# Optimization experiments

Hardware: AMD Instinct MI355X
Metric: run time of the kernel (lower is better)

The kernel has to match this reference:

```python
import jax, jax.numpy as jnp
import numpy as np
import math

B, S, HID, H = 1, 2048, 1024, 16
D = HID // H  # head_dim = 64


def setup_inputs() -> dict:
    key = jax.random.key(0)
    ks = jax.random.split(key, 12)
    s = 0.02
    x = jax.random.normal(ks[0], (B, S, HID), jnp.float32)
    Wq = jax.random.normal(ks[1], (HID, HID), jnp.float32) * s
    bq = jnp.zeros((HID,), jnp.float32)
    Wk = jax.random.normal(ks[2], (HID, HID), jnp.float32) * s
    bk = jnp.zeros((HID,), jnp.float32)
    Wv = jax.random.normal(ks[3], (HID, HID), jnp.float32) * s
    bv = jnp.zeros((HID,), jnp.float32)
    Wo = jax.random.normal(ks[4], (HID, HID), jnp.float32) * s
    bo = jnp.zeros((HID,), jnp.float32)
    # nn.Parameter(torch.ones(3,3)) at init; small noise so the bias is non-degenerate
    cmw = jnp.ones((3, 3), jnp.float32) + 0.1 * jax.random.normal(ks[5], (3, 3), jnp.float32)
    # full causal [B,S,S] mask so the mask.shape[1]==seq_len branch is taken
    mask = jnp.tril(jnp.ones((B, S, S), jnp.int32))
    modality_info = jax.random.randint(ks[6], (B, S), 0, 3, dtype=jnp.int64)
    return dict(x=x, Wq=Wq, bq=bq, Wk=Wk, bk=bk, Wv=Wv, bv=bv, Wo=Wo, bo=bo,
                cmw=cmw, mask=mask, modality_info=modality_info)


def reference(x, Wq, bq, Wk, bk, Wv, bv, Wo, bo, cmw, mask, modality_info):
    b, s, _ = x.shape
    # QKV projections (torch Linear: y = x @ W.T + b), split into heads [B,H,S,D]
    q = (x @ Wq.T + bq).reshape(b, s, H, D).transpose(0, 2, 1, 3)
    k = (x @ Wk.T + bk).reshape(b, s, H, D).transpose(0, 2, 1, 3)
    v = (x @ Wv.T + bv).reshape(b, s, H, D).transpose(0, 2, 1, 3)
    scores = jnp.einsum('bhqd,bhkd->bhqk', q, k) / math.sqrt(D)  # [B,H,S,S]
    # cross-modal bias: gather from 3x3 table via pairwise modality indices -> [B,S,S]
    bias = cmw[modality_info[:, :, None], modality_info[:, None, :]]
    scores = scores + bias[:, None, :, :]  # equals original broadcast when B==1
    scores = jnp.where(mask[:, None, :, :] == 0, -1e9, scores)
    attn = jax.nn.softmax(scores, axis=-1)  # dropout is identity in eval
    ctx = jnp.einsum('bhqk,bhkd->bhqd', attn, v)          # [B,H,S,D]
    ctx = ctx.transpose(0, 2, 1, 3).reshape(b, s, HID)    # [B,S,HID]
    return ctx @ Wo.T + bo
```

## Files before the change

kernel.cpp:

```cpp
#include <hip/hip_runtime.h>
#include <hip/hip_bf16.h>
#include <math.h>

#define S_LEN 2048
#define HID   1024
#define NHEAD 16

using bf16x8 = __attribute__((ext_vector_type(8))) short;
using f32x4  = __attribute__((ext_vector_type(4))) float;

__device__ __forceinline__ float bf2f(short s) {
  union { unsigned u; float f; } c;
  c.u = ((unsigned)(unsigned short)s) << 16;
  return c.f;
}
__device__ __forceinline__ short f2bf(float f) {
  union { float f; unsigned u; } c; c.f = f;
  unsigned u = c.u;
  unsigned r = (u + 0x7fffu + ((u >> 16) & 1u)) >> 16;
  return (short)r;
}
__device__ __forceinline__ float loadf(const void* base, long idx, int is_bf) {
  return is_bf ? bf2f(((const short*)base)[idx]) : ((const float*)base)[idx];
}

__global__ void detect_kernel(const unsigned* __restrict__ xw,
                              const int* __restrict__ modw,
                              int* __restrict__ flags) {
  const int t = threadIdx.x;
  int cnt = 0;
  for (int i = t; i < 1024; i += 64) {
    const unsigned fld = (xw[i] >> 7) & 0xFFu;
    cnt += (fld >= 100u && fld <= 135u) ? 1 : 0;
  }
  int odd = 0;
  for (int i = 0; i < 4; ++i) {
    const int wv = modw[2 * (t + 64 * i) + 1];
    odd += (wv != 0) ? 1 : 0;
  }
  for (int m = 1; m < 64; m <<= 1) {
    cnt += __shfl_xor(cnt, m);
    odd += __shfl_xor(odd, m);
  }
  if (t == 0) {
    flags[0] = (cnt >= 512) ? 1 : 0;
    flags[1] = (odd == 0) ? 1 : 0;
  }
}

__global__ __launch_bounds__(256) void convert5(
    const void* __restrict__ s0, const void* __restrict__ s1, const void* __restrict__ s2,
    const void* __restrict__ s3, const void* __restrict__ s4,
    short* __restrict__ d0, short* __restrict__ d1, short* __restrict__ d2,
    short* __restrict__ d3, short* __restrict__ d4,
    const int* __restrict__ flags) {
  const int a = blockIdx.y;
  const void* src = (a == 0) ? s0 : (a == 1) ? s1 : (a == 2) ? s2 : (a == 3) ? s3 : s4;
  short* dst = (a == 0) ? d0 : (a == 1) ? d1 : (a == 2) ? d2 : (a == 3) ? d3 : d4;
  const long n = (a == 0) ? (2L << 20) : (1L << 20);
  const int is_bf = flags[0];
  long i = (long)(blockIdx.x * 256 + threadIdx.x) * 8;
  const long stride = (long)gridDim.x * 256 * 8;
  if (is_bf) {
    for (; i < n; i += stride)
      *(bf16x8*)(dst + i) = *(const bf16x8*)((const short*)src + i);
  } else {
    for (; i < n; i += stride) {
      const float* p = (const float*)src + i;
      bf16x8 r;
#pragma unroll
      for (int j = 0; j < 8; ++j) r[j] = f2bf(p[j]);
      *(bf16x8*)(dst + i) = r;
    }
  }
}

__global__ __launch_bounds__(256) void gemm_bt3(
    const short* __restrict__ A,
    const short* __restrict__ W0, const short* __restrict__ W1, const short* __restrict__ W2,
    const void* __restrict__ b0, const void* __restrict__ b1, const void* __restrict__ b2,
    void* __restrict__ C0, void* __restrict__ C1, void* __restrict__ C2,
    const int* __restrict__ flags, int nbn, int store_f32)
{
  constexpr int K = 1024;
  constexpr int N = 1024;
  __shared__ short As[128 * 32];
  __shared__ short Bs[128 * 32];

  const int t = threadIdx.x;
  const int w = t >> 6, lane = t & 63;
  const int l15 = lane & 15, quad = lane >> 4;
  const int wm = w >> 1, wn = w & 1;

  const int is_bf = flags[0];
  const int bx = blockIdx.x;
  const int mat = bx / nbn;
  const int n0 = (bx % nbn) * 128;
  const int m0 = blockIdx.y * 128;

  const short* W  = (mat == 0) ? W0 : (mat == 1 ? W1 : W2);
  const void* bia = (mat == 0) ? b0 : (mat == 1 ? b1 : b2);
  void*       C   = (mat == 0) ? C0 : (mat == 1 ? C1 : C2);

  f32x4 acc[4][4];
  for (int mi = 0; mi < 4; ++mi)
    for (int ni = 0; ni < 4; ++ni)
      for (int r = 0; r < 4; ++r) acc[mi][ni][r] = 0.f;

  const int srow = t >> 2;
  const int sch  = (t & 3) * 8;
  const short* Ap = A + (long)(m0 + srow) * K + sch;
  const short* Wp = W + (long)(n0 + srow) * K + sch;

  bf16x8 ra0 = *(const bf16x8*)(Ap);
  bf16x8 ra1 = *(const bf16x8*)(Ap + 64L * K);
  bf16x8 rb0 = *(const bf16x8*)(Wp);
  bf16x8 rb1 = *(const bf16x8*)(Wp + 64L * K);

  for (int kt = 0; kt < K / 32; ++kt) {
    __syncthreads();
    *(bf16x8*)&As[(srow)      * 32 + sch] = ra0;
    *(bf16x8*)&As[(srow + 64) * 32 + sch] = ra1;
    *(bf16x8*)&Bs[(srow)      * 32 + sch] = rb0;
    *(bf16x8*)&Bs[(srow + 64) * 32 + sch] = rb1;
    __syncthreads();
    if (kt + 1 < K / 32) {
      ra0 = *(const bf16x8*)(Ap + (kt + 1) * 32);
      ra1 = *(const bf16x8*)(Ap + (kt + 1) * 32 + 64L * K);
      rb0 = *(const bf16x8*)(Wp + (kt + 1) * 32);
      rb1 = *(const bf16x8*)(Wp + (kt + 1) * 32 + 64L * K);
    }
    bf16x8 af[4], bfr[4];
    for (int mi = 0; mi < 4; ++mi)
      af[mi] = *(const bf16x8*)&As[(wm * 64 + mi * 16 + l15) * 32 + quad * 8];
    for (int ni = 0; ni < 4; ++ni)
      bfr[ni] = *(const bf16x8*)&Bs[(wn * 64 + ni * 16 + l15) * 32 + quad * 8];
    for (int mi = 0; mi < 4; ++mi)
      for (int ni = 0; ni < 4; ++ni)
        acc[mi][ni] = __builtin_amdgcn_mfma_f32_16x16x32_bf16(af[mi], bfr[ni], acc[mi][ni], 0, 0, 0);
  }

  for (int ni = 0; ni < 4; ++ni) {
    const int col = n0 + wn * 64 + ni * 16 + l15;
    const float bv = loadf(bia, col, is_bf);
    for (int mi = 0; mi < 4; ++mi) {
      const int row = m0 + wm * 64 + mi * 16 + quad * 4;
      for (int r = 0; r < 4; ++r) {
        const float v = acc[mi][ni][r] + bv;
        const long idx = (long)(row + r) * N + col;
        if (store_f32) ((float*)C)[idx] = v;
        else           ((short*)C)[idx] = f2bf(v);
      }
    }
  }
}

__global__ __launch_bounds__(256) void attn_kernel(
    const short* __restrict__ Q, const short* __restrict__ Kg, const short* __restrict__ Vg,
    const int* __restrict__ mod, const void* __restrict__ cmw,
    const int* __restrict__ flags, short* __restrict__ CTX)
{
  __shared__ short Ks[64 * 80];
  __shared__ short Vt[64 * 80];
  __shared__ short Ps[4 * 16 * 80];
  __shared__ float cm[9];
  __shared__ int mods[2048];

  const int t = threadIdx.x;
  const int w = t >> 6, lane = t & 63;
  const int l15 = lane & 15, quad = lane >> 4;
  const int h = blockIdx.y;
  const int m64 = flags[1];

  if (t < 9) cm[t] = loadf(cmw, t, flags[0]);
  for (int i = t; i < 2048; i += 256) mods[i] = mod[i << m64];
  __syncthreads();

  const int krow = t >> 3, kch = (t & 7) * 8;
  const int vkp = t & 63, vdc = (t >> 6) * 8;

  for (int half = 0; half < 2; ++half) {
    const int strip = (half == 0) ? (int)blockIdx.x : 31 - (int)blockIdx.x;
    const int q0 = strip * 64;
    const int nkt = strip + 1;

    const short* qb = Q + (long)(q0 + w * 16 + l15) * HID + h * 64 + quad * 8;
    const bf16x8 aq0 = *(const bf16x8*)qb;
    const bf16x8 aq1 = *(const bf16x8*)(qb + 32);

    int mrow[4];
    for (int r = 0; r < 4; ++r) mrow[r] = mods[q0 + w * 16 + quad * 4 + r];

    float m_i[4], l_i[4];
    f32x4 acc_o[4];
    for (int r = 0; r < 4; ++r) { m_i[r] = -1e30f; l_i[r] = 0.f; }
    for (int ni = 0; ni < 4; ++ni)
      for (int r = 0; r < 4; ++r) acc_o[ni][r] = 0.f;

    bf16x8 rk0 = *(const bf16x8*)(Kg + (long)krow * HID + h * 64 + kch);
    bf16x8 rk1 = *(const bf16x8*)(Kg + (long)(krow + 32) * HID + h * 64 + kch);
    bf16x8 rv0 = *(const bf16x8*)(Vg + (long)vkp * HID + h * 64 + vdc);
    bf16x8 rv1 = *(const bf16x8*)(Vg + (long)vkp * HID + h * 64 + 32 + vdc);

    for (int kt = 0; kt < nkt; ++kt) {
      __syncthreads();
      *(bf16x8*)&Ks[krow * 80 + kch] = rk0;
      *(bf16x8*)&Ks[(krow + 32) * 80 + kch] = rk1;
#pragma unroll
      for (int j = 0; j < 8; ++j) Vt[(vdc + j) * 80 + vkp] = rv0[j];
#pragma unroll
      for (int j = 0; j < 8; ++j) Vt[(vdc + 32 + j) * 80 + vkp] = rv1[j];
      __syncthreads();
      if (kt + 1 < nkt) {
        const long kb = (long)((kt + 1) * 64) * HID + h * 64;
        rk0 = *(const bf16x8*)(Kg + kb + (long)krow * HID + kch);
        rk1 = *(const bf16x8*)(Kg + kb + (long)(krow + 32) * HID + kch);
        rv0 = *(const bf16x8*)(Vg + kb + (long)vkp * HID + vdc);
        rv1 = *(const bf16x8*)(Vg + kb + (long)vkp * HID + 32 + vdc);
      }

      f32x4 sc[4];
      for (int nt = 0; nt < 4; ++nt) {
        const bf16x8 kb0 = *(const bf16x8*)&Ks[(nt * 16 + l15) * 80 + quad * 8];
        const bf16x8 kb1 = *(const bf16x8*)&Ks[(nt * 16 + l15) * 80 + 32 + quad * 8];
        f32x4 z;
        for (int r = 0; r < 4; ++r) z[r] = 0.f;
        z = __builtin_amdgcn_mfma_f32_16x16x32_bf16(aq0, kb0, z, 0, 0, 0);
        z = __builtin_amdgcn_mfma_f32_16x16x32_bf16(aq1, kb1, z, 0, 0, 0);
        sc[nt] = z;
      }

      float sv[4][4], rmax[4];
      for (int r = 0; r < 4; ++r) rmax[r] = -1e30f;
      for (int nt = 0; nt < 4; ++nt) {
        const int mcol = mods[kt * 64 + nt * 16 + l15];
        for (int r = 0; r < 4; ++r) {
          float x = sc[nt][r] * 0.125f + cm[mrow[r] * 3 + mcol];
          sv[nt][r] = x;
          rmax[r] = fmaxf(rmax[r], x);
        }
      }
      if (kt == nkt - 1) {
        for (int r = 0; r < 4; ++r) rmax[r] = -1e30f;
        for (int nt = 0; nt < 4; ++nt) {
          const int col = kt * 64 + nt * 16 + l15;
          for (int r = 0; r < 4; ++r) {
            const int row = q0 + w * 16 + quad * 4 + r;
            sv[nt][r] = (col <= row) ? sv[nt][r] : -1e30f;
            rmax[r] = fmaxf(rmax[r], sv[nt][r]);
          }
        }
      }
      for (int off = 1; off < 16; off <<= 1)
        for (int r = 0; r < 4; ++r) rmax[r] = fmaxf(rmax[r], __shfl_xor(rmax[r], off));

      float alpha[4], rsum[4];
      for (int r = 0; r < 4; ++r) {
        const float mn = fmaxf(m_i[r], rmax[r]);
        alpha[r] = __expf(m_i[r] - mn);
        m_i[r] = mn;
        rsum[r] = 0.f;
      }
      short pb[4][4];
      for (int nt = 0; nt < 4; ++nt)
        for (int r = 0; r < 4; ++r) {
          const float p = __expf(sv[nt][r] - m_i[r]);
          rsum[r] += p;
          pb[nt][r] = f2bf(p);
        }
      for (int off = 1; off < 16; off <<= 1)
        for (int r = 0; r < 4; ++r) rsum[r] += __shfl_xor(rsum[r], off);
      for (int r = 0; r < 4; ++r) l_i[r] = l_i[r] * alpha[r] + rsum[r];
      for (int ni = 0; ni < 4; ++ni)
        for (int r = 0; r < 4; ++r) acc_o[ni][r] *= alpha[r];

      short* Pw = &Ps[w * 16 * 80];
      for (int nt = 0; nt < 4; ++nt)
        for (int r = 0; r < 4; ++r)
          Pw[(quad * 4 + r) * 80 + nt * 16 + l15] = pb[nt][r];
      asm volatile("s_waitcnt lgkmcnt(0)" ::: "memory");

      for (int kk = 0; kk < 2; ++kk) {
        const bf16x8 ap = *(const bf16x8*)&Pw[l15 * 80 + kk * 32 + quad * 8];
        for (int ni = 0; ni < 4; ++ni) {
          const bf16x8 bv = *(const bf16x8*)&Vt[(ni * 16 + l15) * 80 + kk * 32 + quad * 8];
          acc_o[ni] = __builtin_amdgcn_mfma_f32_16x16x32_bf16(ap, bv, acc_o[ni], 0, 0, 0);
        }
      }
    }

    for (int ni = 0; ni < 4; ++ni) {
      const int col = h * 64 + ni * 16 + l15;
      for (int r = 0; r < 4; ++r) {
        const int row = q0 + w * 16 + quad * 4 + r;
        CTX[(long)row * HID + col] = f2bf(acc_o[ni][r] / l_i[r]);
      }
    }
  }
}

extern "C" void kernel_launch(void* const* d_in, const int* in_sizes, int n_in,
                              void* d_out, int out_size, void* d_ws, size_t ws_size,
                              hipStream_t stream) {
  constexpr long M1 = 1024L * 1024L;
  int*   flags = (int*)d_ws;
  short* base  = (short*)d_ws + 128;
  short* xb  = base;
  short* Wqb = xb + 2 * M1;
  short* Wkb = Wqb + M1;
  short* Wvb = Wkb + M1;
  short* Wob = Wvb + M1;
  short* Qw  = Wob + M1;
  short* Kw  = Qw + 2 * M1;
  short* Vw  = Kw + 2 * M1;
  short* CTX = Vw + 2 * M1;
  const int* modality = (const int*)d_in[11];

  detect_kernel<<<1, 64, 0, stream>>>((const unsigned*)d_in[0], modality, flags);
  convert5<<<dim3(512, 5), 256, 0, stream>>>(
      d_in[0], d_in[1], d_in[3], d_in[5], d_in[7],
      xb, Wqb, Wkb, Wvb, Wob, flags);

  gemm_bt3<<<dim3(24, 16), 256, 0, stream>>>(
      xb, Wqb, Wkb, Wvb, d_in[2], d_in[4], d_in[6],
      Qw, Kw, Vw, flags, 8, 0);
  attn_kernel<<<dim3(16, NHEAD), 256, 0, stream>>>(Qw, Kw, Vw, modality, d_in[9], flags, CTX);
  gemm_bt3<<<dim3(8, 16), 256, 0, stream>>>(
      CTX, Wob, Wob, Wob, d_in[8], d_in[8], d_in[8],
      d_out, d_out, d_out, flags, 8, 1);
}
```

Before: 206.8 us.

## Split attention KV range across two blocks with merge pass; shrink GEMM N-tile

```diff
diff --git a/kernel.cpp b/kernel.cpp
--- a/kernel.cpp
+++ b/kernel.cpp
@@ -7,6 +7,7 @@
 #define NHEAD 16
 
 using bf16x8 = __attribute__((ext_vector_type(8))) short;
+using bf16x4 = __attribute__((ext_vector_type(4))) short;
 using f32x4  = __attribute__((ext_vector_type(4))) float;
 
 __device__ __forceinline__ float bf2f(short s) {
@@ -85,7 +86,7 @@
   constexpr int K = 1024;
   constexpr int N = 1024;
   __shared__ short As[128 * 32];
-  __shared__ short Bs[128 * 32];
+  __shared__ short Bs[64 * 32];
 
   const int t = threadIdx.x;
   const int w = t >> 6, lane = t & 63;
@@ -95,16 +96,16 @@
   const int is_bf = flags[0];
   const int bx = blockIdx.x;
   const int mat = bx / nbn;
-  const int n0 = (bx % nbn) * 128;
+  const int n0 = (bx % nbn) * 64;
   const int m0 = blockIdx.y * 128;
 
   const short* W  = (mat == 0) ? W0 : (mat == 1 ? W1 : W2);
   const void* bia = (mat == 0) ? b0 : (mat == 1 ? b1 : b2);
   void*       C   = (mat == 0) ? C0 : (mat == 1 ? C1 : C2);
 
-  f32x4 acc[4][4];
+  f32x4 acc[4][2];
   for (int mi = 0; mi < 4; ++mi)
-    for (int ni = 0; ni < 4; ++ni)
+    for (int ni = 0; ni < 2; ++ni)
       for (int r = 0; r < 4; ++r) acc[mi][ni][r] = 0.f;
 
   const int srow = t >> 2;
@@ -115,33 +116,30 @@
   bf16x8 ra0 = *(const bf16x8*)(Ap);
   bf16x8 ra1 = *(const bf16x8*)(Ap + 64L * K);
   bf16x8 rb0 = *(const bf16x8*)(Wp);
-  bf16x8 rb1 = *(const bf16x8*)(Wp + 64L * K);
 
   for (int kt = 0; kt < K / 32; ++kt) {
     __syncthreads();
     *(bf16x8*)&As[(srow)      * 32 + sch] = ra0;
     *(bf16x8*)&As[(srow + 64) * 32 + sch] = ra1;
     *(bf16x8*)&Bs[(srow)      * 32 + sch] = rb0;
-    *(bf16x8*)&Bs[(srow + 64) * 32 + sch] = rb1;
     __syncthreads();
     if (kt + 1 < K / 32) {
       ra0 = *(const bf16x8*)(Ap + (kt + 1) * 32);
       ra1 = *(const bf16x8*)(Ap + (kt + 1) * 32 + 64L * K);
       rb0 = *(const bf16x8*)(Wp + (kt + 1) * 32);
-      rb1 = *(const bf16x8*)(Wp + (kt + 1) * 32 + 64L * K);
-    }
-    bf16x8 af[4], bfr[4];
+    }
+    bf16x8 af[4], bfr[2];
     for (int mi = 0; mi < 4; ++mi)
       af[mi] = *(const bf16x8*)&As[(wm * 64 + mi * 16 + l15) * 32 + quad * 8];
-    for (int ni = 0; ni < 4; ++ni)
-      bfr[ni] = *(const bf16x8*)&Bs[(wn * 64 + ni * 16 + l15) * 32 + quad * 8];
+    for (int ni = 0; ni < 2; ++ni)
+      bfr[ni] = *(const bf16x8*)&Bs[(wn * 32 + ni * 16 + l15) * 32 + quad * 8];
     for (int mi = 0; mi < 4; ++mi)
-      for (int ni = 0; ni < 4; ++ni)
+      for (int ni = 0; ni < 2; ++ni)
         acc[mi][ni] = __builtin_amdgcn_mfma_f32_16x16x32_bf16(af[mi], bfr[ni], acc[mi][ni], 0, 0, 0);
   }
 
-  for (int ni = 0; ni < 4; ++ni) {
-    const int col = n0 + wn * 64 + ni * 16 + l15;
+  for (int ni = 0; ni < 2; ++ni) {
+    const int col = n0 + wn * 32 + ni * 16 + l15;
     const float bv = loadf(bia, col, is_bf);
     for (int mi = 0; mi < 4; ++mi) {
       const int row = m0 + wm * 64 + mi * 16 + quad * 4;
@@ -155,10 +153,11 @@
   }
 }
 
-__global__ __launch_bounds__(256) void attn_kernel(
+__global__ __launch_bounds__(256) void attn_split(
     const short* __restrict__ Q, const short* __restrict__ Kg, const short* __restrict__ Vg,
     const int* __restrict__ mod, const void* __restrict__ cmw,
-    const int* __restrict__ flags, short* __restrict__ CTX)
+    const int* __restrict__ flags,
+    short* __restrict__ PO, float* __restrict__ PM, float* __restrict__ PL)
 {
   __shared__ short Ks[64 * 80];
   __shared__ short Vt[64 * 80];
@@ -170,6 +169,8 @@
   const int w = t >> 6, lane = t & 63;
   const int l15 = lane & 15, quad = lane >> 4;
   const int h = blockIdx.y;
+  const int pair = blockIdx.x >> 1;
+  const int par  = blockIdx.x & 1;
   const int m64 = flags[1];
 
   if (t < 9) cm[t] = loadf(cmw, t, flags[0]);
@@ -179,8 +180,8 @@
   const int krow = t >> 3, kch = (t & 7) * 8;
   const int vkp = t & 63, vdc = (t >> 6) * 8;
 
-  for (int half = 0; half < 2; ++half) {
-    const int strip = (half == 0) ? (int)blockIdx.x : 31 - (int)blockIdx.x;
+  for (int si = 0; si < 2; ++si) {
+    const int strip = (si == 0) ? pair : 31 - pair;
     const int q0 = strip * 64;
     const int nkt = strip + 1;
 
@@ -197,12 +198,16 @@
     for (int ni = 0; ni < 4; ++ni)
       for (int r = 0; r < 4; ++r) acc_o[ni][r] = 0.f;
 
-    bf16x8 rk0 = *(const bf16x8*)(Kg + (long)krow * HID + h * 64 + kch);
-    bf16x8 rk1 = *(const bf16x8*)(Kg + (long)(krow + 32) * HID + h * 64 + kch);
-    bf16x8 rv0 = *(const bf16x8*)(Vg + (long)vkp * HID + h * 64 + vdc);
-    bf16x8 rv1 = *(const bf16x8*)(Vg + (long)vkp * HID + h * 64 + 32 + vdc);
-
-    for (int kt = 0; kt < nkt; ++kt) {
+    bf16x8 rk0, rk1, rv0, rv1;
+    if (par < nkt) {
+      const long kb = (long)(par * 64) * HID + h * 64;
+      rk0 = *(const bf16x8*)(Kg + kb + (long)krow * HID + kch);
+      rk1 = *(const bf16x8*)(Kg + kb + (long)(krow + 32) * HID + kch);
+      rv0 = *(const bf16x8*)(Vg + kb + (long)vkp * HID + vdc);
+      rv1 = *(const bf16x8*)(Vg + kb + (long)vkp * HID + 32 + vdc);
+    }
+
+    for (int kt = par; kt < nkt; kt += 2) {
       __syncthreads();
       *(bf16x8*)&Ks[krow * 80 + kch] = rk0;
       *(bf16x8*)&Ks[(krow + 32) * 80 + kch] = rk1;
@@ -211,8 +216,8 @@
 #pragma unroll
       for (int j = 0; j < 8; ++j) Vt[(vdc + 32 + j) * 80 + vkp] = rv1[j];
       __syncthreads();
-      if (kt + 1 < nkt) {
-        const long kb = (long)((kt + 1) * 64) * HID + h * 64;
+      if (kt + 2 < nkt) {
+        const long kb = (long)((kt + 2) * 64) * HID + h * 64;
         rk0 = *(const bf16x8*)(Kg + kb + (long)krow * HID + kch);
         rk1 = *(const bf16x8*)(Kg + kb + (long)(krow + 32) * HID + kch);
         rv0 = *(const bf16x8*)(Vg + kb + (long)vkp * HID + vdc);
@@ -289,14 +294,45 @@
       }
     }
 
+    const long pbase = (long)par * 2097152;
     for (int ni = 0; ni < 4; ++ni) {
       const int col = h * 64 + ni * 16 + l15;
       for (int r = 0; r < 4; ++r) {
         const int row = q0 + w * 16 + quad * 4 + r;
-        CTX[(long)row * HID + col] = f2bf(acc_o[ni][r] / l_i[r]);
-      }
-    }
-  }
+        PO[pbase + (long)row * HID + col] = f2bf(acc_o[ni][r]);
+      }
+    }
+    if (l15 == 0) {
+      for (int r = 0; r < 4; ++r) {
+        const int row = q0 + w * 16 + quad * 4 + r;
+        PM[par * 32768 + row * 16 + h] = m_i[r];
+        PL[par * 32768 + row * 16 + h] = l_i[r];
+      }
+    }
+  }
+}
+
+__global__ __launch_bounds__(256) void attn_merge(
+    const short* __restrict__ PO, const float* __restrict__ PM, const float* __restrict__ PL,
+    short* __restrict__ CTX)
+{
+  const int row = blockIdx.x;
+  const int t = threadIdx.x;
+  const int h = t >> 4;
+  const int d0 = (t & 15) * 4;
+  const float m0 = PM[row * 16 + h], m1 = PM[32768 + row * 16 + h];
+  const float l0 = PL[row * 16 + h], l1 = PL[32768 + row * 16 + h];
+  const float M = fmaxf(m0, m1);
+  const float w0 = __expf(m0 - M), w1 = __expf(m1 - M);
+  const float inv = 1.f / (l0 * w0 + l1 * w1);
+  const long b = (long)row * HID + h * 64 + d0;
+  const bf16x4 o0 = *(const bf16x4*)&PO[b];
+  const bf16x4 o1 = *(const bf16x4*)&PO[2097152 + b];
+  bf16x4 out;
+#pragma unroll
+  for (int j = 0; j < 4; ++j)
+    out[j] = f2bf((bf2f(o0[j]) * w0 + bf2f(o1[j]) * w1) * inv);
+  *(bf16x4*)&CTX[b] = out;
 }
 
 extern "C" void kernel_launch(void* const* d_in, const int* in_sizes, int n_in,
@@ -314,6 +350,9 @@
   short* Kw  = Qw + 2 * M1;
   short* Vw  = Kw + 2 * M1;
   short* CTX = Vw + 2 * M1;
+  short* PO = xb;
+  float* PM = (float*)Wvb;
+  float* PL = PM + 65536;
   const int* modality = (const int*)d_in[11];
 
   detect_kernel<<<1, 64, 0, stream>>>((const unsigned*)d_in[0], modality, flags);
@@ -321,11 +360,13 @@
       d_in[0], d_in[1], d_in[3], d_in[5], d_in[7],
       xb, Wqb, Wkb, Wvb, Wob, flags);
 
-  gemm_bt3<<<dim3(24, 16), 256, 0, stream>>>(
+  gemm_bt3<<<dim3(48, 16), 256, 0, stream>>>(
       xb, Wqb, Wkb, Wvb, d_in[2], d_in[4], d_in[6],
-      Qw, Kw, Vw, flags, 8, 0);
-  attn_kernel<<<dim3(16, NHEAD), 256, 0, stream>>>(Qw, Kw, Vw, modality, d_in[9], flags, CTX);
-  gemm_bt3<<<dim3(8, 16), 256, 0, stream>>>(
+      Qw, Kw, Vw, flags, 16, 0);
+  attn_split<<<dim3(32, NHEAD), 256, 0, stream>>>(
+      Qw, Kw, Vw, modality, d_in[9], flags, PO, PM, PL);
+  attn_merge<<<dim3(S_LEN), 256, 0, stream>>>(PO, PM, PL, CTX);
+  gemm_bt3<<<dim3(16, 16), 256, 0, stream>>>(
       CTX, Wob, Wob, Wob, d_in[8], d_in[8], d_in[8],
-      d_out, d_out, d_out, flags, 8, 1);
-}
+      d_out, d_out, d_out, flags, 16, 1);
+}
```

Result: faster. 190.4 us (-7.9%).
